# Performance work log

Measured on AMD Instinct MI355X. Metric: run time of the kernel, lower is better.

## Reference

```python
import jax, jax.numpy as jnp
import numpy as np

N = 100000
E = 1600000
IN_FEATS = 256
HID = 128


def _graph_conv(x, W, b, src, dst, n_nodes):
    # DGL GraphConv with norm='both':
    #   out = D_in^{-1/2} * A * (D_out^{-1/2} * x @ W) + b
    ones = jnp.ones(src.shape[0], dtype=x.dtype)
    deg_out = jax.ops.segment_sum(ones, src, num_segments=n_nodes)
    deg_in = jax.ops.segment_sum(ones, dst, num_segments=n_nodes)
    norm_src = jnp.maximum(deg_out, 1.0) ** -0.5  # [N]
    norm_dst = jnp.maximum(deg_in, 1.0) ** -0.5   # [N]
    h = (x * norm_src[:, None]) @ W               # [N, HID]
    msg = h[src]                                  # [E, HID] gather
    agg = jax.ops.segment_sum(msg, dst, num_segments=n_nodes)  # [N, HID] scatter-add
    return agg * norm_dst[:, None] + b


def setup_inputs() -> dict:
    key = jax.random.key(0)
    ks = jax.random.split(key, 12)
    x = jax.random.normal(ks[0], (N, IN_FEATS), dtype=jnp.float32)
    src0 = jax.random.randint(ks[1], (E,), 0, N, dtype=jnp.int32)
    dst0 = jax.random.randint(ks[2], (E,), 0, N, dtype=jnp.int32)
    src1 = jax.random.randint(ks[3], (E,), 0, N, dtype=jnp.int32)
    dst1 = jax.random.randint(ks[4], (E,), 0, N, dtype=jnp.int32)
    s_e = 1.0 / np.sqrt(IN_FEATS)
    s_h = 1.0 / np.sqrt(HID)
    We = jax.random.uniform(ks[5], (IN_FEATS, HID), jnp.float32, -s_e, s_e)
    be = jax.random.uniform(ks[6], (HID,), jnp.float32, -s_e, s_e)
    W1 = jax.random.uniform(ks[7], (HID, HID), jnp.float32, -s_h, s_h)
    b1 = jnp.zeros((HID,), jnp.float32)
    W2 = jax.random.uniform(ks[8], (HID, HID), jnp.float32, -s_h, s_h)
    b2 = jnp.zeros((HID,), jnp.float32)
    return {"x": x, "We": We, "be": be, "W1": W1, "b1": b1, "W2": W2, "b2": b2,
            "src0": src0, "dst0": dst0, "src1": src1, "dst1": dst1}


def reference(x, We, be, W1, b1, W2, b2, src0, dst0, src1, dst1):
    n = x.shape[0]
    h = x @ We + be                                   # embed
    h = jax.nn.relu(_graph_conv(h, W1, b1, src0, dst0, n))
    h = jax.nn.relu(_graph_conv(h, W2, b2, src1, dst1, n))
    return h
```

## Files before the change

kernel.cpp:

```cpp
#include <hip/hip_runtime.h>

#define HID 128
#define NBUCK 512
#define BSHIFT 8
#define NB 512
#define M4 (4 * NBUCK * NB)
#define STAGE_CAP 8192
#define PCAP 7168

typedef __attribute__((ext_vector_type(8))) short bf16x8;
typedef __attribute__((ext_vector_type(4))) float f32x4;

__device__ __forceinline__ unsigned short f2bf(float f) {
    union { float f; unsigned u; } v; v.f = f;
    unsigned r = v.u + 0x7fff + ((v.u >> 16) & 1);
    return (unsigned short)(r >> 16);
}
__device__ __forceinline__ float bf2f(unsigned short b) {
    union { float f; unsigned u; } v; v.u = ((unsigned)b) << 16;
    return v.f;
}

__device__ __forceinline__ void gload_lds16(const void* g, void* l) {
    __builtin_amdgcn_global_load_lds(
        (const __attribute__((address_space(1))) void*)g,
        (__attribute__((address_space(3))) void*)l, 16, 0, 0);
}

__global__ __launch_bounds__(256) void bucket_count_all(
    const int* __restrict__ k0, const int* __restrict__ k1,
    const int* __restrict__ k2, const int* __restrict__ k3,
    int* __restrict__ counts, int E, int chunk) {
    __shared__ int h[4][NBUCK];
    int tid = threadIdx.x;
    #pragma unroll
    for (int j = 0; j < 8; ++j) ((int*)h)[tid + j * 256] = 0;
    __syncthreads();
    int base = blockIdx.x * chunk;
    int end = min(base + chunk, E);
    const int* keys[4] = {k0, k1, k2, k3};
    #pragma unroll
    for (int p = 0; p < 4; ++p) {
        const int* kp = keys[p];
        for (int i = base + tid; i < end; i += 256)
            atomicAdd(&h[p][kp[i] >> BSHIFT], 1);
    }
    __syncthreads();
    #pragma unroll
    for (int p = 0; p < 4; ++p) {
        counts[((p << 9) + tid) * NB + blockIdx.x] = h[p][tid];
        counts[((p << 9) + tid + 256) * NB + blockIdx.x] = h[p][tid + 256];
    }
}

__global__ __launch_bounds__(256) void scan_a(int* __restrict__ data, int* __restrict__ partials, int m) {
    __shared__ int sdata[256];
    int base = blockIdx.x * 1024;
    int tid = threadIdx.x;
    int v[4]; int s = 0;
    #pragma unroll
    for (int i = 0; i < 4; ++i) { int idx = base + tid * 4 + i; v[i] = (idx < m) ? data[idx] : 0; s += v[i]; }
    sdata[tid] = s; __syncthreads();
    for (int off = 1; off < 256; off <<= 1) {
        int t = (tid >= off) ? sdata[tid - off] : 0; __syncthreads();
        sdata[tid] += t; __syncthreads();
    }
    int excl = sdata[tid] - s;
    if (tid == 255) partials[blockIdx.x] = sdata[255];
    int run = excl;
    #pragma unroll
    for (int i = 0; i < 4; ++i) { int idx = base + tid * 4 + i; if (idx < m) data[idx] = run; run += v[i]; }
}

__global__ __launch_bounds__(1024) void scan_b(int* __restrict__ partials, int nb) {
    __shared__ int sdata[1024];
    int tid = threadIdx.x;
    int v = (tid < nb) ? partials[tid] : 0;
    sdata[tid] = v; __syncthreads();
    for (int off = 1; off < 1024; off <<= 1) {
        int t = (tid >= off) ? sdata[tid - off] : 0; __syncthreads();
        sdata[tid] += t; __syncthreads();
    }
    if (tid < nb) partials[tid] = sdata[tid] - v;
}

__global__ __launch_bounds__(256) void scan_c(int* __restrict__ data, const int* __restrict__ partials, int m) {
    int i = blockIdx.x * 256 + threadIdx.x;
    if (i < m) data[i] += partials[i >> 10];
}

__global__ __launch_bounds__(256) void bucket_scatter_all(
    const int* __restrict__ k0, const int* __restrict__ k1,
    const int* __restrict__ k2, const int* __restrict__ k3,
    const int* __restrict__ pay0, const int* __restrict__ pay1,
    const int* __restrict__ scanned, unsigned* __restrict__ bucketed,
    int E, int chunk) {
    __shared__ unsigned cur[4][NBUCK];
    int tid = threadIdx.x;
    int blk = blockIdx.x;
    #pragma unroll
    for (int p = 0; p < 4; ++p) {
        cur[p][tid]       = (unsigned)scanned[((p << 9) + tid) * NB + blk];
        cur[p][tid + 256] = (unsigned)scanned[((p << 9) + tid + 256) * NB + blk];
    }
    __syncthreads();
    int base = blk * chunk;
    int end = min(base + chunk, E);
    const int* keys[4] = {k0, k1, k2, k3};
    const int* pays[4] = {pay0, pay1, nullptr, nullptr};
    #pragma unroll
    for (int p = 0; p < 4; ++p) {
        const int* kp = keys[p];
        const int* pp = pays[p];
        for (int i = base + tid; i < end; i += 256) {
            int k = kp[i];
            int b = k >> BSHIFT;
            unsigned pay = pp ? (unsigned)pp[i] : 0u;
            unsigned pos = atomicAdd(&cur[p][b], 1u);
            bucketed[pos] = ((unsigned)(k & 255) << 17) | pay;
        }
    }
}

__global__ __launch_bounds__(256) void bucket_finalize(
    const unsigned* __restrict__ bucketed, const int* __restrict__ scanned,
    int* __restrict__ prow0, int* __restrict__ prow1,
    int* __restrict__ din0, int* __restrict__ din1,
    int* __restrict__ dout0, int* __restrict__ dout1,
    int* __restrict__ csr0, int* __restrict__ csr1, int n, int E) {
    __shared__ unsigned stage[STAGE_CAP];
    __shared__ int cnt[256];
    __shared__ int sd[256];
    __shared__ int pexcl[256];
    __shared__ int cur[256];
    int tid = threadIdx.x;
    int g = blockIdx.x;
    int p = g >> 9;
    int b = g & 511;
    int start = scanned[g * NB];
    int end = (g == 4 * NBUCK - 1) ? 4 * E : scanned[(g + 1) * NB];
    if (end - start > STAGE_CAP) end = start + STAGE_CAP;
    int len = end - start;
    int node0 = b << BSHIFT;

    cnt[tid] = 0;
    __syncthreads();
    if (p < 2) {
        for (int i = tid; i < len; i += 256) {
            unsigned v = bucketed[start + i];
            stage[i] = v;
            atomicAdd(&cnt[v >> 17], 1);
        }
    } else {
        for (int i = tid; i < len; i += 256)
            atomicAdd(&cnt[bucketed[start + i] >> 17], 1);
    }
    __syncthreads();

    if (p >= 2) {
        int* dout = (p == 2) ? dout0 : dout1;
        int node = node0 + tid;
        if (node < n) dout[node] = cnt[tid];
        return;
    }

    int c = cnt[tid];
    int pc = (c + 15) & ~15;
    sd[tid] = pc;
    __syncthreads();
    for (int off = 1; off < 256; off <<= 1) {
        int t = (tid >= off) ? sd[tid - off] : 0; __syncthreads();
        sd[tid] += t; __syncthreads();
    }
    pexcl[tid] = sd[tid] - pc;
    cur[tid] = 0;
    __syncthreads();
    int ptot = sd[255];
    if (ptot > PCAP) ptot = PCAP;

    int* csr  = (p == 0) ? csr0  : csr1;
    int* prow = (p == 0) ? prow0 : prow1;
    int* din  = (p == 0) ? din0  : din1;
    int node = node0 + tid;
    if (node < n) { prow[node] = b * PCAP + pexcl[tid]; din[node] = c; }

    const int base = b * PCAP;
    for (int j = tid; j < ptot; j += 256) csr[base + j] = n;
    __syncthreads();
    for (int i = tid; i < len; i += 256) {
        unsigned w = stage[i];
        int nl = (int)(w >> 17);
        int pos = base + pexcl[nl] + atomicAdd(&cur[nl], 1);
        csr[pos] = (int)(w & 0x1FFFFu);
    }
}

__device__ __forceinline__ size_t bswz_idx(int k, int col) {
    int s = k >> 5, lh = (k >> 3) & 3, j = k & 7;
    int c = col >> 4, lc = col & 15;
    return ((((size_t)s * 8 + c) * 64 + (lh * 16 + lc)) * 8 + j);
}

__global__ __launch_bounds__(256) void weight_fuse(
    const float* __restrict__ We, const float* __restrict__ be,
    const float* __restrict__ W1,
    unsigned short* __restrict__ B1h, unsigned short* __restrict__ B1l,
    float* __restrict__ cv) {
    __shared__ float w1[128][128];
    int tid = threadIdx.x;
    #pragma unroll
    for (int it = 0; it < 16; ++it) {
        int s = tid + it * 256;
        int r = s >> 5, c4 = (s & 31) << 2;
        *(float4*)&w1[r][c4] = *(const float4*)&W1[r * 128 + c4];
    }
    __syncthreads();
    int j = tid & 127;
    int half = tid >> 7;
    if (blockIdx.x == 128) {
        if (half) return;
        float sum = 0.f;
        for (int k = 0; k < 128; ++k) sum += be[k] * w1[k][j];
        cv[j] = sum;
        return;
    }
    int i = blockIdx.x * 2 + half;
    const float* arow = &We[i * 128];
    float sum = 0.f;
    for (int k = 0; k < 128; ++k) sum += arow[k] * w1[k][j];
    unsigned short h = f2bf(sum);
    unsigned short l = f2bf(sum - bf2f(h));
    size_t o = bswz_idx(i, j);
    B1h[o] = h; B1l[o] = l;
}

__global__ __launch_bounds__(256) void swizzle_split(
    const float* __restrict__ W, unsigned short* __restrict__ Bh,
    unsigned short* __restrict__ Bl, int K) {
    int idx = blockIdx.x * 256 + threadIdx.x;
    if (idx >= K * 128) return;
    int k = idx >> 7, col = idx & 127;
    float v = W[idx];
    unsigned short h = f2bf(v);
    unsigned short l = f2bf(v - bf2f(h));
    size_t o = bswz_idx(k, col);
    Bh[o] = h; Bl[o] = l;
}

template <int K, bool AFP32>
__global__ __launch_bounds__(512) void gemm_lds(
    const void* __restrict__ X_,
    const unsigned short* __restrict__ Bh, const unsigned short* __restrict__ Bl,
    const float* __restrict__ cvec, const int* __restrict__ degs,
    unsigned short* __restrict__ T, int n) {
    constexpr int NS = K / 32;
    __shared__ __align__(16) char smem[2 * 16384];
    const int tid = threadIdx.x;
    const int wave = tid >> 6;
    const int lane = tid & 63;
    const int lr = lane & 15;
    const int lk = lane >> 4;
    const int row0 = blockIdx.x * 128 + wave * 16;
    const int grow = row0 + lr;
    const bool vr = grow < n;

    f32x4 acc[8];
    #pragma unroll
    for (int c = 0; c < 8; ++c) acc[c] = (f32x4)0.f;

    auto stage_slab = [&](int s, char* dst) {
        #pragma unroll
        for (int it = 0; it < 2; ++it) {
            int u = tid + it * 512;
            int f = u >> 6;
            int c = f >> 1, plane = f & 1;
            const unsigned short* srcArr = plane ? Bl : Bh;
            const char* g = (const char*)srcArr +
                ((size_t)(s * 512 + c * 64 + (u & 63)) * 16);
            gload_lds16(g, dst + u * 16);
        }
    };

    stage_slab(0, smem);

    const float* pxf = AFP32 ? (const float*)X_ + (size_t)grow * K + lk * 8 : nullptr;
    const unsigned short* pxb = AFP32 ? nullptr : (const unsigned short*)X_ + (size_t)grow * K + lk * 8;
    float4 a0 = make_float4(0.f, 0.f, 0.f, 0.f), a1 = a0;
    bf16x8 ab = (bf16x8)0;
    if (AFP32) {
        if (vr) { a0 = *(const float4*)pxf; a1 = *(const float4*)(pxf + 4); }
    } else {
        if (vr) ab = *(const bf16x8*)pxb;
    }

    #pragma unroll
    for (int s = 0; s < NS; ++s) {
        __syncthreads();
        if (s + 1 < NS) stage_slab(s + 1, smem + ((s + 1) & 1) * 16384);

        float4 n0 = make_float4(0.f, 0.f, 0.f, 0.f), n1 = n0;
        bf16x8 nb = (bf16x8)0;
        if (s + 1 < NS && vr) {
            if (AFP32) {
                n0 = *(const float4*)(pxf + (s + 1) * 32);
                n1 = *(const float4*)(pxf + (s + 1) * 32 + 4);
            } else {
                nb = *(const bf16x8*)(pxb + (s + 1) * 32);
            }
        }

        bf16x8 ah, al;
        if (AFP32) {
            float av[8] = {a0.x, a0.y, a0.z, a0.w, a1.x, a1.y, a1.z, a1.w};
            #pragma unroll
            for (int j = 0; j < 8; ++j) {
                unsigned short h = f2bf(av[j]);
                ah[j] = (short)h;
                al[j] = (short)f2bf(av[j] - bf2f(h));
            }
        } else {
            ah = ab;
        }

        const char* base = smem + (s & 1) * 16384 + lane * 16;
        #pragma unroll
        for (int c = 0; c < 8; ++c) {
            bf16x8 bh = *(const bf16x8*)(base + (c * 2) * 1024);
            bf16x8 bl = *(const bf16x8*)(base + (c * 2 + 1) * 1024);
            acc[c] = __builtin_amdgcn_mfma_f32_16x16x32_bf16(ah, bh, acc[c], 0, 0, 0);
            acc[c] = __builtin_amdgcn_mfma_f32_16x16x32_bf16(ah, bl, acc[c], 0, 0, 0);
            if (AFP32)
                acc[c] = __builtin_amdgcn_mfma_f32_16x16x32_bf16(al, bh, acc[c], 0, 0, 0);
        }
        a0 = n0; a1 = n1; ab = nb;
    }

    #pragma unroll
    for (int r = 0; r < 4; ++r) {
        int orow = row0 + lk * 4 + r;
        if (orow >= n) continue;
        float norm = rsqrtf(fmaxf((float)degs[orow], 1.0f));
        #pragma unroll
        for (int c = 0; c < 8; ++c) {
            float v = acc[c][r];
            if (cvec) v += cvec[c * 16 + lr];
            T[(size_t)orow * 128 + c * 16 + lr] = f2bf(v * norm);
        }
    }
}

template <bool OUT_BF16>
__global__ __launch_bounds__(256) void aggregate(
    const unsigned short* __restrict__ T, const int* __restrict__ prow,
    const int* __restrict__ din, const int* __restrict__ csr,
    const float* __restrict__ bias, void* __restrict__ out_, int n) {
    const int wave = threadIdx.x >> 6;
    const int lane = threadIdx.x & 63;
    const int half = lane >> 5;
    const int l32 = lane & 31;
    const int node = blockIdx.x * 4 + wave;
    if (node >= n) return;
    const int beg = prow[node];
    const int d = din[node];
    const int plen = (d + 15) & ~15;
    float a0 = 0.f, a1 = 0.f, a2 = 0.f, a3 = 0.f;
    for (int e = beg; e < beg + plen; e += 16) {
        int sidx[8];
        #pragma unroll
        for (int j = 0; j < 8; ++j) sidx[j] = csr[e + j * 2 + half];
        #pragma unroll
        for (int j = 0; j < 8; ++j) {
            uint2 u = *(const uint2*)&T[(size_t)sidx[j] * 128 + l32 * 4];
            a0 += __uint_as_float(u.x << 16);
            a1 += __uint_as_float(u.x & 0xffff0000u);
            a2 += __uint_as_float(u.y << 16);
            a3 += __uint_as_float(u.y & 0xffff0000u);
        }
    }
    a0 += __shfl_xor(a0, 32);
    a1 += __shfl_xor(a1, 32);
    a2 += __shfl_xor(a2, 32);
    a3 += __shfl_xor(a3, 32);
    if (half == 0) {
        float norm = rsqrtf(fmaxf((float)d, 1.0f));
        float4 bv = *(const float4*)&bias[l32 * 4];
        float o0 = fmaxf(a0 * norm + bv.x, 0.f);
        float o1 = fmaxf(a1 * norm + bv.y, 0.f);
        float o2 = fmaxf(a2 * norm + bv.z, 0.f);
        float o3 = fmaxf(a3 * norm + bv.w, 0.f);
        if (OUT_BF16) {
            unsigned w0 = (unsigned)f2bf(o0) | ((unsigned)f2bf(o1) << 16);
            unsigned w1 = (unsigned)f2bf(o2) | ((unsigned)f2bf(o3) << 16);
            uint2* dst = (uint2*)((unsigned short*)out_ + (size_t)node * 128 + l32 * 4);
            *dst = make_uint2(w0, w1);
        } else {
            float4* dst = (float4*)((float*)out_ + (size_t)node * 128 + l32 * 4);
            *dst = make_float4(o0, o1, o2, o3);
        }
    }
}

extern "C" void kernel_launch(void* const* d_in, const int* in_sizes, int n_in,
                              void* d_out, int out_size, void* d_ws, size_t ws_size,
                              hipStream_t stream) {
    const float* x   = (const float*)d_in[0];
    const float* We  = (const float*)d_in[1];
    const float* be  = (const float*)d_in[2];
    const float* W1  = (const float*)d_in[3];
    const float* b1  = (const float*)d_in[4];
    const float* W2  = (const float*)d_in[5];
    const float* b2  = (const float*)d_in[6];
    const int* src0  = (const int*)d_in[7];
    const int* dst0  = (const int*)d_in[8];
    const int* src1  = (const int*)d_in[9];
    const int* dst1  = (const int*)d_in[10];
    float* out = (float*)d_out;

    const int n = in_sizes[0] / 256;
    const int E = in_sizes[7];
    const int chunk = (E + NB - 1) / NB;

    char* p = (char*)d_ws;
    auto carve = [&](size_t bytes) -> void* {
        void* r = (void*)p;
        p += (bytes + 511) & ~(size_t)511;
        return r;
    };
    unsigned short* t        = (unsigned short*)carve(((size_t)n + 1) * HID * 2);
    unsigned*       bucketed = (unsigned*)carve((size_t)4 * E * 4);
    int*            counts   = (int*)carve((size_t)M4 * 4);
    int*            partials = (int*)carve(1024 * 4);
    int*            csr0     = (int*)carve((size_t)NBUCK * PCAP * 4);
    int*            csr1     = (int*)carve((size_t)NBUCK * PCAP * 4);
    int*            prow0    = (int*)carve((size_t)n * 4);
    int*            prow1    = (int*)carve((size_t)n * 4);
    int*            din0     = (int*)carve((size_t)n * 4);
    int*            din1     = (int*)carve((size_t)n * 4);
    int*            dout0    = (int*)carve((size_t)n * 4);
    int*            dout1    = (int*)carve((size_t)n * 4);
    unsigned short* B1h      = (unsigned short*)carve(256 * HID * 2);
    unsigned short* B1l      = (unsigned short*)carve(256 * HID * 2);
    unsigned short* B2h      = (unsigned short*)carve(128 * HID * 2);
    unsigned short* B2l      = (unsigned short*)carve(128 * HID * 2);
    float*          cv       = (float*)carve(HID * 4);

    unsigned short* h1 = (unsigned short*)bucketed;

    const int gGemm  = (n + 127) / 128;
    const int gAggN  = (n + 3) / 4;
    const int gScanA = (M4 + 1023) / 1024;
    const int gScanC = (M4 + 255) / 256;

    hipMemsetAsync(t + (size_t)n * HID, 0, HID * 2, stream);

    bucket_count_all<<<NB, 256, 0, stream>>>(dst0, dst1, src0, src1, counts, E, chunk);
    scan_a<<<gScanA, 256, 0, stream>>>(counts, partials, M4);
    scan_b<<<1, 1024, 0, stream>>>(partials, gScanA);
    scan_c<<<gScanC, 256, 0, stream>>>(counts, partials, M4);
    bucket_scatter_all<<<NB, 256, 0, stream>>>(dst0, dst1, src0, src1, src0, src1,
                                               counts, bucketed, E, chunk);
    bucket_finalize<<<4 * NBUCK, 256, 0, stream>>>(bucketed, counts, prow0, prow1,
                                                   din0, din1, dout0, dout1, csr0, csr1, n, E);

    weight_fuse<<<129, 256, 0, stream>>>(We, be, W1, B1h, B1l, cv);
    swizzle_split<<<(128 * 128 + 255) / 256, 256, 0, stream>>>(W2, B2h, B2l, 128);

    gemm_lds<256, true><<<gGemm, 512, 0, stream>>>((const void*)x, B1h, B1l, cv, dout0, t, n);
    aggregate<true><<<gAggN, 256, 0, stream>>>(t, prow0, din0, csr0, b1, (void*)h1, n);
    gemm_lds<128, false><<<gGemm, 512, 0, stream>>>((const void*)h1, B2h, B2l, nullptr, dout1, t, n);
    aggregate<false><<<gAggN, 256, 0, stream>>>(t, prow1, din1, csr1, b2, (void*)out, n);
}
```

Before: 306.7 us.

## Make GEMMs persistent with fully LDS-resident weights and column-group split

Replaces the per-block double-buffered weight-slab GEMM with a persistent kernel. Each of 512 blocks loads its whole weight slice into LDS once, then grid-strides over 16-row tiles, which removes the repeated weight staging and the per-slab barriers. For the first GEMM (K=256) the columns are split into two groups of 64 across alternating blocks so the weights fit in LDS (64KB). The cost is that X rows are read twice in the first GEMM, and occupancy is lower because of the large LDS footprint and the fixed grid.

```diff
diff --git a/kernel.cpp b/kernel.cpp
--- a/kernel.cpp
+++ b/kernel.cpp
@@ -247,104 +247,114 @@
     Bh[o] = h; Bl[o] = l;
 }
 
-template <int K, bool AFP32>
-__global__ __launch_bounds__(512) void gemm_lds(
+template <int K, bool AFP32, int GROUPS>
+__global__ __launch_bounds__(512) void gemm_stream(
     const void* __restrict__ X_,
     const unsigned short* __restrict__ Bh, const unsigned short* __restrict__ Bl,
     const float* __restrict__ cvec, const int* __restrict__ degs,
     unsigned short* __restrict__ T, int n) {
     constexpr int NS = K / 32;
-    __shared__ __align__(16) char smem[2 * 16384];
+    constexpr int NC = 8 / GROUPS;
+    constexpr int LOG2NC = (NC == 4) ? 2 : 3;
+    constexpr int LDSB = NS * NC * 2 * 1024;
+    __shared__ __align__(16) char smem[LDSB];
     const int tid = threadIdx.x;
     const int wave = tid >> 6;
     const int lane = tid & 63;
     const int lr = lane & 15;
     const int lk = lane >> 4;
-    const int row0 = blockIdx.x * 128 + wave * 16;
-    const int grow = row0 + lr;
-    const bool vr = grow < n;
-
-    f32x4 acc[8];
-    #pragma unroll
-    for (int c = 0; c < 8; ++c) acc[c] = (f32x4)0.f;
-
-    auto stage_slab = [&](int s, char* dst) {
+    const int colgroup = (GROUPS == 2) ? (int)(blockIdx.x & 1) : 0;
+    const int bstripe  = (GROUPS == 2) ? (int)(blockIdx.x >> 1) : (int)blockIdx.x;
+    const int nstripes = (GROUPS == 2) ? (int)(gridDim.x >> 1) : (int)gridDim.x;
+
+    constexpr int TOT16 = LDSB / 16;
+    #pragma unroll
+    for (int it = 0; it < TOT16 / 512; ++it) {
+        int u = tid + it * 512;
+        int f = u >> 6;
+        int plane = f & 1;
+        int sc = f >> 1;
+        int c = sc & (NC - 1);
+        int s = sc >> LOG2NC;
+        const unsigned short* srcArr = plane ? Bl : Bh;
+        const char* gsrc = (const char*)srcArr +
+            ((size_t)(s * 512 + (colgroup * NC + c) * 64 + (u & 63)) * 16);
+        gload_lds16(gsrc, smem + (size_t)u * 16);
+    }
+    __syncthreads();
+
+    const int tilesTotal = (n + 15) >> 4;
+    for (int rt = bstripe * 8 + wave; rt < tilesTotal; rt += nstripes * 8) {
+        const int row0 = rt << 4;
+        const int grow = row0 + lr;
+        const bool vr = grow < n;
+
+        f32x4 acc[NC];
         #pragma unroll
-        for (int it = 0; it < 2; ++it) {
-            int u = tid + it * 512;
-            int f = u >> 6;
-            int c = f >> 1, plane = f & 1;
-            const unsigned short* srcArr = plane ? Bl : Bh;
-            const char* g = (const char*)srcArr +
-                ((size_t)(s * 512 + c * 64 + (u & 63)) * 16);
-            gload_lds16(g, dst + u * 16);
-        }
-    };
-
-    stage_slab(0, smem);
-
-    const float* pxf = AFP32 ? (const float*)X_ + (size_t)grow * K + lk * 8 : nullptr;
-    const unsigned short* pxb = AFP32 ? nullptr : (const unsigned short*)X_ + (size_t)grow * K + lk * 8;
-    float4 a0 = make_float4(0.f, 0.f, 0.f, 0.f), a1 = a0;
-    bf16x8 ab = (bf16x8)0;
-    if (AFP32) {
-        if (vr) { a0 = *(const float4*)pxf; a1 = *(const float4*)(pxf + 4); }
-    } else {
-        if (vr) ab = *(const bf16x8*)pxb;
-    }
-
-    #pragma unroll
-    for (int s = 0; s < NS; ++s) {
-        __syncthreads();
-        if (s + 1 < NS) stage_slab(s + 1, smem + ((s + 1) & 1) * 16384);
-
-        float4 n0 = make_float4(0.f, 0.f, 0.f, 0.f), n1 = n0;
-        bf16x8 nb = (bf16x8)0;
-        if (s + 1 < NS && vr) {
+        for (int c = 0; c < NC; ++c) acc[c] = (f32x4)0.f;
+
+        const float* pxf = (const float*)X_ + (size_t)grow * K + lk * 8;
+        const unsigned short* pxb = (const unsigned short*)X_ + (size_t)grow * K + lk * 8;
+
+        float4 a0 = make_float4(0.f, 0.f, 0.f, 0.f), a1 = a0;
+        bf16x8 ab = (bf16x8)0;
+        if (AFP32) {
+            if (vr) { a0 = *(const float4*)pxf; a1 = *(const float4*)(pxf + 4); }
+        } else {
+            if (vr) ab = *(const bf16x8*)pxb;
+        }
+
+        const char* base = smem + lane * 16;
+        #pragma unroll
+        for (int s = 0; s < NS; ++s) {
+            float4 n0 = make_float4(0.f, 0.f, 0.f, 0.f), n1 = n0;
+            bf16x8 nb = (bf16x8)0;
+            if (s + 1 < NS && vr) {
+                if (AFP32) {
+                    n0 = *(const float4*)(pxf + (s + 1) * 32);
+                    n1 = *(const float4*)(pxf + (s + 1) * 32 + 4);
+                } else {
+                    nb = *(const bf16x8*)(pxb + (s + 1) * 32);
+                }
+            }
+
+            bf16x8 ah, al;
             if (AFP32) {
-                n0 = *(const float4*)(pxf + (s + 1) * 32);
-                n1 = *(const float4*)(pxf + (s + 1) * 32 + 4);
+                float av[8] = {a0.x, a0.y, a0.z, a0.w, a1.x, a1.y, a1.z, a1.w};
+                #pragma unroll
+                for (int j = 0; j < 8; ++j) {
+                    unsigned short h = f2bf(av[j]);
+                    ah[j] = (short)h;
+                    al[j] = (short)f2bf(av[j] - bf2f(h));
+                }
             } else {
-                nb = *(const bf16x8*)(pxb + (s + 1) * 32);
+                ah = ab;
             }
-        }
-
-        bf16x8 ah, al;
-        if (AFP32) {
-            float av[8] = {a0.x, a0.y, a0.z, a0.w, a1.x, a1.y, a1.z, a1.w};
+
             #pragma unroll
-            for (int j = 0; j < 8; ++j) {
-                unsigned short h = f2bf(av[j]);
-                ah[j] = (short)h;
-                al[j] = (short)f2bf(av[j] - bf2f(h));
+            for (int c = 0; c < NC; ++c) {
+                bf16x8 bh = *(const bf16x8*)(base + ((s * NC + c) * 2) * 1024);
+                bf16x8 bl = *(const bf16x8*)(base + ((s * NC + c) * 2 + 1) * 1024);
+                acc[c] = __builtin_amdgcn_mfma_f32_16x16x32_bf16(ah, bh, acc[c], 0, 0, 0);
+                acc[c] = __builtin_amdgcn_mfma_f32_16x16x32_bf16(ah, bl, acc[c], 0, 0, 0);
+                if (AFP32)
+                    acc[c] = __builtin_amdgcn_mfma_f32_16x16x32_bf16(al, bh, acc[c], 0, 0, 0);
             }
-        } else {
-            ah = ab;
-        }
-
-        const char* base = smem + (s & 1) * 16384 + lane * 16;
+            a0 = n0; a1 = n1; ab = nb;
+        }
+
         #pragma unroll
-        for (int c = 0; c < 8; ++c) {
-            bf16x8 bh = *(const bf16x8*)(base + (c * 2) * 1024);
-            bf16x8 bl = *(const bf16x8*)(base + (c * 2 + 1) * 1024);
-            acc[c] = __builtin_amdgcn_mfma_f32_16x16x32_bf16(ah, bh, acc[c], 0, 0, 0);
-            acc[c] = __builtin_amdgcn_mfma_f32_16x16x32_bf16(ah, bl, acc[c], 0, 0, 0);
-            if (AFP32)
-                acc[c] = __builtin_amdgcn_mfma_f32_16x16x32_bf16(al, bh, acc[c], 0, 0, 0);
-        }
-        a0 = n0; a1 = n1; ab = nb;
-    }
-
-    #pragma unroll
-    for (int r = 0; r < 4; ++r) {
-        int orow = row0 + lk * 4 + r;
-        if (orow >= n) continue;
-        float norm = rsqrtf(fmaxf((float)degs[orow], 1.0f));
-        #pragma unroll
-        for (int c = 0; c < 8; ++c) {
-            float v = acc[c][r];
-            if (cvec) v += cvec[c * 16 + lr];
-            T[(size_t)orow * 128 + c * 16 + lr] = f2bf(v * norm);
+        for (int r = 0; r < 4; ++r) {
+            int orow = row0 + lk * 4 + r;
+            if (orow >= n) continue;
+            float norm = rsqrtf(fmaxf((float)degs[orow], 1.0f));
+            #pragma unroll
+            for (int c = 0; c < NC; ++c) {
+                int col = (colgroup * NC + c) * 16 + lr;
+                float v = acc[c][r];
+                if (cvec) v += cvec[col];
+                T[(size_t)orow * 128 + col] = f2bf(v * norm);
+            }
         }
     }
 }
@@ -446,7 +456,6 @@
 
     unsigned short* h1 = (unsigned short*)bucketed;
 
-    const int gGemm  = (n + 127) / 128;
     const int gAggN  = (n + 3) / 4;
     const int gScanA = (M4 + 1023) / 1024;
     const int gScanC = (M4 + 255) / 256;
@@ -465,8 +474,8 @@
     weight_fuse<<<129, 256, 0, stream>>>(We, be, W1, B1h, B1l, cv);
     swizzle_split<<<(128 * 128 + 255) / 256, 256, 0, stream>>>(W2, B2h, B2l, 128);
 
-    gemm_lds<256, true><<<gGemm, 512, 0, stream>>>((const void*)x, B1h, B1l, cv, dout0, t, n);
+    gemm_stream<256, true, 2><<<512, 512, 0, stream>>>((const void*)x, B1h, B1l, cv, dout0, t, n);
     aggregate<true><<<gAggN, 256, 0, stream>>>(t, prow0, din0, csr0, b1, (void*)h1, n);
-    gemm_lds<128, false><<<gGemm, 512, 0, stream>>>((const void*)h1, B2h, B2l, nullptr, dout1, t, n);
+    gemm_stream<128, false, 1><<<512, 512, 0, stream>>>((const void*)h1, B2h, B2l, nullptr, dout1, t, n);
     aggregate<false><<<gAggN, 256, 0, stream>>>(t, prow1, din1, csr1, b2, (void*)out, n);
 }
```

Result: slower. 435.6 us (+42.0%).

## Triple-buffer GEMM weight slabs with prefetch distance two and explicit vmcnt waits

Applied to the files above, without the earlier changes.

Moves the GEMM's LDS staging of weight slabs and the A-row register prefetch from double to triple buffering, issuing loads two stages ahead. The full __syncthreads is replaced by explicit s_waitcnt vmcnt counts plus a raw s_barrier. Out-of-range rows are clamped to the last valid row instead of being predicated, so loads are never skipped. This is meant to hide more global-load latency behind the MFMAs, at the cost of 48KB of LDS per block and fragile hand-tuned vmcnt values that depend on how many loads the compiler emits.

```diff
diff --git a/kernel.cpp b/kernel.cpp
--- a/kernel.cpp
+++ b/kernel.cpp
@@ -254,7 +254,7 @@
     const float* __restrict__ cvec, const int* __restrict__ degs,
     unsigned short* __restrict__ T, int n) {
     constexpr int NS = K / 32;
-    __shared__ __align__(16) char smem[2 * 16384];
+    __shared__ __align__(16) char smem[3 * 16384];
     const int tid = threadIdx.x;
     const int wave = tid >> 6;
     const int lane = tid & 63;
@@ -262,13 +262,14 @@
     const int lk = lane >> 4;
     const int row0 = blockIdx.x * 128 + wave * 16;
     const int grow = row0 + lr;
-    const bool vr = grow < n;
+    const int growc = (grow < n) ? grow : (n - 1);
 
     f32x4 acc[8];
     #pragma unroll
     for (int c = 0; c < 8; ++c) acc[c] = (f32x4)0.f;
 
-    auto stage_slab = [&](int s, char* dst) {
+    auto stage_slab = [&](int s) {
+        char* dst = smem + (s % 3) * 16384;
         #pragma unroll
         for (int it = 0; it < 2; ++it) {
             int u = tid + it * 512;
@@ -281,36 +282,47 @@
         }
     };
 
-    stage_slab(0, smem);
-
-    const float* pxf = AFP32 ? (const float*)X_ + (size_t)grow * K + lk * 8 : nullptr;
-    const unsigned short* pxb = AFP32 ? nullptr : (const unsigned short*)X_ + (size_t)grow * K + lk * 8;
-    float4 a0 = make_float4(0.f, 0.f, 0.f, 0.f), a1 = a0;
-    bf16x8 ab = (bf16x8)0;
-    if (AFP32) {
-        if (vr) { a0 = *(const float4*)pxf; a1 = *(const float4*)(pxf + 4); }
-    } else {
-        if (vr) ab = *(const bf16x8*)pxb;
+    const float* pxf = (const float*)X_ + (size_t)growc * K + lk * 8;
+    const unsigned short* pxb = (const unsigned short*)X_ + (size_t)growc * K + lk * 8;
+
+    float4 af0[3], af1[3];
+    bf16x8 abv[3];
+    #pragma unroll
+    for (int i = 0; i < 3; ++i) {
+        af0[i] = make_float4(0.f, 0.f, 0.f, 0.f);
+        af1[i] = af0[i];
+        abv[i] = (bf16x8)0;
+    }
+
+    stage_slab(0);
+    if (AFP32) { af0[0] = *(const float4*)(pxf); af1[0] = *(const float4*)(pxf + 4); }
+    else       { abv[0] = *(const bf16x8*)(pxb); }
+    stage_slab(1);
+    if (NS > 1) {
+        if (AFP32) { af0[1] = *(const float4*)(pxf + 32); af1[1] = *(const float4*)(pxf + 32 + 4); }
+        else       { abv[1] = *(const bf16x8*)(pxb + 32); }
     }
 
     #pragma unroll
     for (int s = 0; s < NS; ++s) {
-        __syncthreads();
-        if (s + 1 < NS) stage_slab(s + 1, smem + ((s + 1) & 1) * 16384);
-
-        float4 n0 = make_float4(0.f, 0.f, 0.f, 0.f), n1 = n0;
-        bf16x8 nb = (bf16x8)0;
-        if (s + 1 < NS && vr) {
+        if (AFP32) asm volatile("s_waitcnt vmcnt(4)" ::: "memory");
+        else       asm volatile("s_waitcnt vmcnt(3)" ::: "memory");
+        __builtin_amdgcn_sched_barrier(0);
+        __builtin_amdgcn_s_barrier();
+
+        if (s + 2 < NS) {
+            stage_slab(s + 2);
             if (AFP32) {
-                n0 = *(const float4*)(pxf + (s + 1) * 32);
-                n1 = *(const float4*)(pxf + (s + 1) * 32 + 4);
+                af0[(s + 2) % 3] = *(const float4*)(pxf + (s + 2) * 32);
+                af1[(s + 2) % 3] = *(const float4*)(pxf + (s + 2) * 32 + 4);
             } else {
-                nb = *(const bf16x8*)(pxb + (s + 1) * 32);
+                abv[(s + 2) % 3] = *(const bf16x8*)(pxb + (s + 2) * 32);
             }
         }
 
         bf16x8 ah, al;
         if (AFP32) {
+            const float4 a0 = af0[s % 3], a1 = af1[s % 3];
             float av[8] = {a0.x, a0.y, a0.z, a0.w, a1.x, a1.y, a1.z, a1.w};
             #pragma unroll
             for (int j = 0; j < 8; ++j) {
@@ -319,10 +331,10 @@
                 al[j] = (short)f2bf(av[j] - bf2f(h));
             }
         } else {
-            ah = ab;
-        }
-
-        const char* base = smem + (s & 1) * 16384 + lane * 16;
+            ah = abv[s % 3];
+        }
+
+        const char* base = smem + (s % 3) * 16384 + lane * 16;
         #pragma unroll
         for (int c = 0; c < 8; ++c) {
             bf16x8 bh = *(const bf16x8*)(base + (c * 2) * 1024);
@@ -332,7 +344,6 @@
             if (AFP32)
                 acc[c] = __builtin_amdgcn_mfma_f32_16x16x32_bf16(al, bh, acc[c], 0, 0, 0);
         }
-        a0 = n0; a1 = n1; ab = nb;
     }
 
     #pragma unroll
```

Result: no change. 310.9 us (+1.4%).

## Double GEMM rows per wave to reuse LDS weight tiles and merge weight prep kernels

Applied to the files above, without the earlier changes.

Each wave of the LDS GEMM now computes two 16-row tiles (256 rows per block), so every B fragment read from LDS feeds twice as many MFMAs and fewer blocks each stage the weight slabs. The weight fusion and W2 swizzle-split kernels are merged into one launch to save a kernel launch. This doubles accumulator registers (64 floats per lane) and halves the grid to about 391 blocks, which may lower occupancy and leave parts of the GPU underused.

```diff
diff --git a/kernel.cpp b/kernel.cpp
--- a/kernel.cpp
+++ b/kernel.cpp
@@ -201,13 +201,25 @@
     return ((((size_t)s * 8 + c) * 64 + (lh * 16 + lc)) * 8 + j);
 }
 
-__global__ __launch_bounds__(256) void weight_fuse(
+__global__ __launch_bounds__(256) void weight_prep(
     const float* __restrict__ We, const float* __restrict__ be,
-    const float* __restrict__ W1,
+    const float* __restrict__ W1, const float* __restrict__ W2,
     unsigned short* __restrict__ B1h, unsigned short* __restrict__ B1l,
+    unsigned short* __restrict__ B2h, unsigned short* __restrict__ B2l,
     float* __restrict__ cv) {
+    int tid = threadIdx.x;
+    if (blockIdx.x >= 129) {
+        int idx = (blockIdx.x - 129) * 256 + tid;
+        if (idx >= 128 * 128) return;
+        int k = idx >> 7, col = idx & 127;
+        float v = W2[idx];
+        unsigned short h = f2bf(v);
+        unsigned short l = f2bf(v - bf2f(h));
+        size_t o = bswz_idx(k, col);
+        B2h[o] = h; B2l[o] = l;
+        return;
+    }
     __shared__ float w1[128][128];
-    int tid = threadIdx.x;
     #pragma unroll
     for (int it = 0; it < 16; ++it) {
         int s = tid + it * 256;
@@ -232,19 +244,6 @@
     unsigned short l = f2bf(sum - bf2f(h));
     size_t o = bswz_idx(i, j);
     B1h[o] = h; B1l[o] = l;
-}
-
-__global__ __launch_bounds__(256) void swizzle_split(
-    const float* __restrict__ W, unsigned short* __restrict__ Bh,
-    unsigned short* __restrict__ Bl, int K) {
-    int idx = blockIdx.x * 256 + threadIdx.x;
-    if (idx >= K * 128) return;
-    int k = idx >> 7, col = idx & 127;
-    float v = W[idx];
-    unsigned short h = f2bf(v);
-    unsigned short l = f2bf(v - bf2f(h));
-    size_t o = bswz_idx(k, col);
-    Bh[o] = h; Bl[o] = l;
 }
 
 template <int K, bool AFP32>
@@ -260,13 +259,16 @@
     const int lane = tid & 63;
     const int lr = lane & 15;
     const int lk = lane >> 4;
-    const int row0 = blockIdx.x * 128 + wave * 16;
-    const int grow = row0 + lr;
-    const bool vr = grow < n;
-
-    f32x4 acc[8];
-    #pragma unroll
-    for (int c = 0; c < 8; ++c) acc[c] = (f32x4)0.f;
+    const int row0 = blockIdx.x * 256 + wave * 32;
+    const int r0 = row0 + lr;
+    const int r1 = row0 + 16 + lr;
+    const bool v0 = r0 < n, v1 = r1 < n;
+
+    f32x4 acc[2][8];
+    #pragma unroll
+    for (int t = 0; t < 2; ++t)
+        #pragma unroll
+        for (int c = 0; c < 8; ++c) acc[t][c] = (f32x4)0.f;
 
     auto stage_slab = [&](int s, char* dst) {
         #pragma unroll
@@ -283,14 +285,19 @@
 
     stage_slab(0, smem);
 
-    const float* pxf = AFP32 ? (const float*)X_ + (size_t)grow * K + lk * 8 : nullptr;
-    const unsigned short* pxb = AFP32 ? nullptr : (const unsigned short*)X_ + (size_t)grow * K + lk * 8;
-    float4 a0 = make_float4(0.f, 0.f, 0.f, 0.f), a1 = a0;
-    bf16x8 ab = (bf16x8)0;
+    const float* pxf0 = (const float*)X_ + (size_t)r0 * K + lk * 8;
+    const float* pxf1 = (const float*)X_ + (size_t)r1 * K + lk * 8;
+    const unsigned short* pxb0 = (const unsigned short*)X_ + (size_t)r0 * K + lk * 8;
+    const unsigned short* pxb1 = (const unsigned short*)X_ + (size_t)r1 * K + lk * 8;
+
+    float4 a00 = make_float4(0.f, 0.f, 0.f, 0.f), a01 = a00, a10 = a00, a11 = a00;
+    bf16x8 ab0 = (bf16x8)0, ab1 = (bf16x8)0;
     if (AFP32) {
-        if (vr) { a0 = *(const float4*)pxf; a1 = *(const float4*)(pxf + 4); }
+        if (v0) { a00 = *(const float4*)pxf0; a01 = *(const float4*)(pxf0 + 4); }
+        if (v1) { a10 = *(const float4*)pxf1; a11 = *(const float4*)(pxf1 + 4); }
     } else {
-        if (vr) ab = *(const bf16x8*)pxb;
+        if (v0) ab0 = *(const bf16x8*)pxb0;
+        if (v1) ab1 = *(const bf16x8*)pxb1;
     }
 
     #pragma unroll
@@ -298,28 +305,34 @@
         __syncthreads();
         if (s + 1 < NS) stage_slab(s + 1, smem + ((s + 1) & 1) * 16384);
 
-        float4 n0 = make_float4(0.f, 0.f, 0.f, 0.f), n1 = n0;
-        bf16x8 nb = (bf16x8)0;
-        if (s + 1 < NS && vr) {
+        float4 n00 = make_float4(0.f, 0.f, 0.f, 0.f), n01 = n00, n10 = n00, n11 = n00;
+        bf16x8 nb0 = (bf16x8)0, nb1 = (bf16x8)0;
+        if (s + 1 < NS) {
             if (AFP32) {
-                n0 = *(const float4*)(pxf + (s + 1) * 32);
-                n1 = *(const float4*)(pxf + (s + 1) * 32 + 4);
+                if (v0) { n00 = *(const float4*)(pxf0 + (s + 1) * 32); n01 = *(const float4*)(pxf0 + (s + 1) * 32 + 4); }
+                if (v1) { n10 = *(const float4*)(pxf1 + (s + 1) * 32); n11 = *(const float4*)(pxf1 + (s + 1) * 32 + 4); }
             } else {
-                nb = *(const bf16x8*)(pxb + (s + 1) * 32);
+                if (v0) nb0 = *(const bf16x8*)(pxb0 + (s + 1) * 32);
+                if (v1) nb1 = *(const bf16x8*)(pxb1 + (s + 1) * 32);
             }
         }
 
-        bf16x8 ah, al;
+        bf16x8 ah[2], al[2];
         if (AFP32) {
-            float av[8] = {a0.x, a0.y, a0.z, a0.w, a1.x, a1.y, a1.z, a1.w};
+            float av0[8] = {a00.x, a00.y, a00.z, a00.w, a01.x, a01.y, a01.z, a01.w};
+            float av1[8] = {a10.x, a10.y, a10.z, a10.w, a11.x, a11.y, a11.z, a11.w};
             #pragma unroll
             for (int j = 0; j < 8; ++j) {
-                unsigned short h = f2bf(av[j]);
-                ah[j] = (short)h;
-                al[j] = (short)f2bf(av[j] - bf2f(h));
+                unsigned short h0 = f2bf(av0[j]);
+                ah[0][j] = (short)h0;
+                al[0][j] = (short)f2bf(av0[j] - bf2f(h0));
+                unsigned short h1 = f2bf(av1[j]);
+                ah[1][j] = (short)h1;
+                al[1][j] = (short)f2bf(av1[j] - bf2f(h1));
             }
         } else {
-            ah = ab;
+            ah[0] = ab0; ah[1] = ab1;
+            al[0] = (bf16x8)0; al[1] = (bf16x8)0;
         }
 
         const char* base = smem + (s & 1) * 16384 + lane * 16;
@@ -327,24 +340,30 @@
         for (int c = 0; c < 8; ++c) {
             bf16x8 bh = *(const bf16x8*)(base + (c * 2) * 1024);
             bf16x8 bl = *(const bf16x8*)(base + (c * 2 + 1) * 1024);
-            acc[c] = __builtin_amdgcn_mfma_f32_16x16x32_bf16(ah, bh, acc[c], 0, 0, 0);
-            acc[c] = __builtin_amdgcn_mfma_f32_16x16x32_bf16(ah, bl, acc[c], 0, 0, 0);
-            if (AFP32)
-                acc[c] = __builtin_amdgcn_mfma_f32_16x16x32_bf16(al, bh, acc[c], 0, 0, 0);
-        }
-        a0 = n0; a1 = n1; ab = nb;
-    }
-
-    #pragma unroll
-    for (int r = 0; r < 4; ++r) {
-        int orow = row0 + lk * 4 + r;
-        if (orow >= n) continue;
-        float norm = rsqrtf(fmaxf((float)degs[orow], 1.0f));
-        #pragma unroll
-        for (int c = 0; c < 8; ++c) {
-            float v = acc[c][r];
-            if (cvec) v += cvec[c * 16 + lr];
-            T[(size_t)orow * 128 + c * 16 + lr] = f2bf(v * norm);
+            #pragma unroll
+            for (int t = 0; t < 2; ++t) {
+                acc[t][c] = __builtin_amdgcn_mfma_f32_16x16x32_bf16(ah[t], bh, acc[t][c], 0, 0, 0);
+                acc[t][c] = __builtin_amdgcn_mfma_f32_16x16x32_bf16(ah[t], bl, acc[t][c], 0, 0, 0);
+                if (AFP32)
+                    acc[t][c] = __builtin_amdgcn_mfma_f32_16x16x32_bf16(al[t], bh, acc[t][c], 0, 0, 0);
+            }
+        }
+        a00 = n00; a01 = n01; a10 = n10; a11 = n11; ab0 = nb0; ab1 = nb1;
+    }
+
+    #pragma unroll
+    for (int t = 0; t < 2; ++t) {
+        #pragma unroll
+        for (int r = 0; r < 4; ++r) {
+            int orow = row0 + t * 16 + lk * 4 + r;
+            if (orow >= n) continue;
+            float norm = rsqrtf(fmaxf((float)degs[orow], 1.0f));
+            #pragma unroll
+            for (int c = 0; c < 8; ++c) {
+                float v = acc[t][c][r];
+                if (cvec) v += cvec[c * 16 + lr];
+                T[(size_t)orow * 128 + c * 16 + lr] = f2bf(v * norm);
+            }
         }
     }
 }
@@ -446,7 +465,7 @@
 
     unsigned short* h1 = (unsigned short*)bucketed;
 
-    const int gGemm  = (n + 127) / 128;
+    const int gGemm  = (n + 255) / 256;
     const int gAggN  = (n + 3) / 4;
     const int gScanA = (M4 + 1023) / 1024;
     const int gScanC = (M4 + 255) / 256;
@@ -462,8 +481,7 @@
     bucket_finalize<<<4 * NBUCK, 256, 0, stream>>>(bucketed, counts, prow0, prow1,
                                                    din0, din1, dout0, dout1, csr0, csr1, n, E);
 
-    weight_fuse<<<129, 256, 0, stream>>>(We, be, W1, B1h, B1l, cv);
-    swizzle_split<<<(128 * 128 + 255) / 256, 256, 0, stream>>>(W2, B2h, B2l, 128);
+    weight_prep<<<193, 256, 0, stream>>>(We, be, W1, W2, B1h, B1l, B2h, B2l, cv);
 
     gemm_lds<256, true><<<gGemm, 512, 0, stream>>>((const void*)x, B1h, B1l, cv, dout0, t, n);
     aggregate<true><<<gAggN, 256, 0, stream>>>(t, prow0, din0, csr0, b1, (void*)h1, n);
```

Result: slower. 316.5 us (+3.2%).
